# Kernel optimization log

Hardware: AMD Instinct MI355X
Metric: run time of the kernel (lower is better)

The kernel has to match this reference:

```python
import jax, jax.numpy as jnp
import numpy as np

EPS = 1e-8
THRESHOLD = 0.5  # ternary quantization threshold

IN_FEATURES = 4096
OUT_FEATURES = 4096


def setup_inputs() -> dict:
    key = jax.random.key(0)
    k_x, k_w, k_b = jax.random.split(key, 3)
    x = jax.random.normal(k_x, (2, 2048, IN_FEATURES), dtype=jnp.float32)
    # xavier_uniform init for weight (out, in)
    limit = float(np.sqrt(6.0 / (IN_FEATURES + OUT_FEATURES)))
    weight = jax.random.uniform(k_w, (OUT_FEATURES, IN_FEATURES), dtype=jnp.float32,
                                minval=-limit, maxval=limit)
    bias = jnp.zeros((OUT_FEATURES,), dtype=jnp.float32)
    return {"x": x, "weight": weight, "bias": bias}


def ternary_quantize(w):
    # scale = mean(|w|), clamped; quantize to {-1,0,1} with 0.5 threshold
    scale = jnp.maximum(jnp.mean(jnp.abs(w)), EPS)
    w_norm = w / scale
    q = jnp.sign(w_norm) * (jnp.abs(w_norm) > THRESHOLD).astype(w.dtype)
    return q, scale


def reference(x, weight, bias):
    # eval-mode forward of BitNetLinear (ternary mode, activation scaling on)
    qw, scale = ternary_quantize(weight)
    input_scale = jnp.maximum(jnp.mean(jnp.abs(x)), EPS)
    scaled_x = x / input_scale
    # F.linear: y = x @ W^T + b, with dequantized weight qw*scale
    out = jnp.einsum('bsi,oi->bso', scaled_x, qw * scale) + bias
    return out * input_scale
```

## Files before the change

### kernel.cpp

```cpp
#include <hip/hip_runtime.h>
#include <hip/hip_bf16.h>

#define AS1 __attribute__((address_space(1)))
#define AS3 __attribute__((address_space(3)))

typedef __attribute__((ext_vector_type(8))) short bfrag8;
typedef __attribute__((ext_vector_type(4))) float floatx4;

static constexpr int M = 4096, N = 4096, K = 4096;
static constexpr long long NELEM = 16777216LL;
static constexpr int PB = 1024;

__device__ __forceinline__ unsigned short f2bf(float f) {
    unsigned int u = __float_as_uint(f);
    u += 0x7FFFu + ((u >> 16) & 1u);
    return (unsigned short)(u >> 16);
}

__device__ __forceinline__ unsigned short tq(float v, float scale_f) {
    float wn = v / scale_f;
    if (fabsf(wn) > 0.5f)
        return (unsigned short)(0x3F80u | ((__float_as_uint(v) >> 16) & 0x8000u));
    return 0;
}

__device__ __forceinline__ double block_reduce(double s) {
    #pragma unroll
    for (int off = 32; off > 0; off >>= 1) s += __shfl_down(s, off, 64);
    __shared__ double part[4];
    int lane = threadIdx.x & 63, wv = threadIdx.x >> 6;
    if (lane == 0) part[wv] = s;
    __syncthreads();
    return part[0] + part[1] + part[2] + part[3];
}

__device__ __forceinline__ void block_reduce2_bcast(double& a, double& b) {
    #pragma unroll
    for (int off = 32; off > 0; off >>= 1) {
        a += __shfl_down(a, off, 64);
        b += __shfl_down(b, off, 64);
    }
    __shared__ double pa[4], pb[4];
    int lane = threadIdx.x & 63, wv = threadIdx.x >> 6;
    if (lane == 0) { pa[wv] = a; pb[wv] = b; }
    __syncthreads();
    a = pa[0] + pa[1] + pa[2] + pa[3];
    b = pb[0] + pb[1] + pb[2] + pb[3];
}

__global__ __launch_bounds__(256) void prep_reduce(
        const float* __restrict__ x, unsigned short* __restrict__ xb,
        const float* __restrict__ w,
        double* __restrict__ px, double* __restrict__ pw) {
    const int b = blockIdx.x;
    const bool isW = b >= PB;
    const int rb = isW ? b - PB : b;
    const float4* src = (const float4*)(isW ? w : x);
    const long long base = (long long)rb * 4096 + threadIdx.x;

    float4 v[16];
    #pragma unroll
    for (int i = 0; i < 16; i++) v[i] = src[base + i * 256];

    double s = 0.0;
    #pragma unroll
    for (int i = 0; i < 16; i++) {
        s += (double)fabsf(v[i].x); s += (double)fabsf(v[i].y);
        s += (double)fabsf(v[i].z); s += (double)fabsf(v[i].w);
    }

    if (!isW) {
        ushort4* xb4 = (ushort4*)xb;
        #pragma unroll
        for (int i = 0; i < 16; i++) {
            ushort4 r;
            r.x = f2bf(v[i].x); r.y = f2bf(v[i].y);
            r.z = f2bf(v[i].z); r.w = f2bf(v[i].w);
            xb4[base + i * 256] = r;
        }
    }

    double bs = block_reduce(s);
    if (threadIdx.x == 0) (isW ? pw : px)[rb] = bs;
}

__global__ __launch_bounds__(256) void quantize_w(
        const float* __restrict__ w, unsigned short* __restrict__ qb,
        const double* __restrict__ px, const double* __restrict__ pw,
        float* __restrict__ scales) {
    const int t = threadIdx.x;
    double sx = 0.0, sw = 0.0;
    #pragma unroll
    for (int i = 0; i < 4; i++) { sx += px[t + i * 256]; sw += pw[t + i * 256]; }
    block_reduce2_bcast(sx, sw);
    const float scale_w = (float)fmax(sw / (double)NELEM, 1e-8);
    const float scale_x = (float)fmax(sx / (double)NELEM, 1e-8);
    if (blockIdx.x == 0 && t == 0) { scales[0] = scale_w; scales[1] = scale_x; }

    const float4* w4 = (const float4*)w;
    ushort4* q4 = (ushort4*)qb;
    const long long base = (long long)blockIdx.x * 4096 + t;
    float4 v[16];
    #pragma unroll
    for (int i = 0; i < 16; i++) v[i] = w4[base + i * 256];
    #pragma unroll
    for (int i = 0; i < 16; i++) {
        ushort4 r;
        r.x = tq(v[i].x, scale_w); r.y = tq(v[i].y, scale_w);
        r.z = tq(v[i].z, scale_w); r.w = tq(v[i].w, scale_w);
        q4[base + i * 256] = r;
    }
}

__global__ __launch_bounds__(256) void gemm_bt(
        const unsigned short* __restrict__ A,
        const unsigned short* __restrict__ B,
        const float* __restrict__ bias,
        const float* __restrict__ scales,
        float* __restrict__ out) {
    __shared__ unsigned short lds[2 * 128 * 64];
    const char* ldsA = (const char*)lds;
    const char* ldsB = (const char*)lds + 16384;

    const int tid = threadIdx.x;
    const int lane = tid & 63;
    const int wv = tid >> 6;
    const int wm = wv & 1;
    const int wn = wv >> 1;
    const int col16 = lane & 15;
    const int quad = lane >> 4;

    const int m0 = blockIdx.y * 128;
    const int n0 = blockIdx.x * 128;

    const int srow = lane >> 3;
    const int scol = ((lane & 7) ^ srow) * 8;

    floatx4 acc[4][4];
    #pragma unroll
    for (int i = 0; i < 4; i++)
        #pragma unroll
        for (int j = 0; j < 4; j++)
            acc[i][j] = (floatx4)0.0f;

    for (int k0 = 0; k0 < K; k0 += 64) {
        #pragma unroll
        for (int j = 0; j < 4; j++) {
            const int c = wv * 4 + j;
            const int row = c * 8 + srow;
            const unsigned short* ga = A + (size_t)(m0 + row) * K + k0 + scol;
            const unsigned short* gb = B + (size_t)(n0 + row) * K + k0 + scol;
            char* la = (char*)lds + c * 1024 + lane * 16;
            char* lb = (char*)lds + 16384 + c * 1024 + lane * 16;
            __builtin_amdgcn_global_load_lds((const AS1 void*)ga, (AS3 void*)la, 16, 0, 0);
            __builtin_amdgcn_global_load_lds((const AS1 void*)gb, (AS3 void*)lb, 16, 0, 0);
        }
        __syncthreads();

        #pragma unroll
        for (int kk = 0; kk < 64; kk += 32) {
            const int kc = (kk >> 3) + quad;
            const int sw = (kc ^ (col16 & 7)) << 4;
            bfrag8 af[4], bfr[4];
            #pragma unroll
            for (int i = 0; i < 4; i++) {
                const int ra = wm * 64 + i * 16 + col16;
                const int rb = wn * 64 + i * 16 + col16;
                af[i]  = *(const bfrag8*)(ldsA + ra * 128 + sw);
                bfr[i] = *(const bfrag8*)(ldsB + rb * 128 + sw);
            }
            #pragma unroll
            for (int i = 0; i < 4; i++)
                #pragma unroll
                for (int j = 0; j < 4; j++)
                    acc[i][j] = __builtin_amdgcn_mfma_f32_16x16x32_bf16(af[i], bfr[j], acc[i][j], 0, 0, 0);
        }
        __syncthreads();
    }

    const float wscale = scales[0];
    const float iscale = scales[1];

    float bv[4];
    #pragma unroll
    for (int j = 0; j < 4; j++)
        bv[j] = bias[n0 + wn * 64 + j * 16 + col16] * iscale;

    #pragma unroll
    for (int i = 0; i < 4; i++) {
        const int mbase = m0 + wm * 64 + i * 16 + quad * 4;
        #pragma unroll
        for (int j = 0; j < 4; j++) {
            const int n = n0 + wn * 64 + j * 16 + col16;
            #pragma unroll
            for (int r = 0; r < 4; r++)
                out[(size_t)(mbase + r) * N + n] = acc[i][j][r] * wscale + bv[j];
        }
    }
}

extern "C" void kernel_launch(void* const* d_in, const int* in_sizes, int n_in,
                              void* d_out, int out_size, void* d_ws, size_t ws_size,
                              hipStream_t stream) {
    const float* x    = (const float*)d_in[0];
    const float* w    = (const float*)d_in[1];
    const float* bias = (const float*)d_in[2];
    float* out = (float*)d_out;

    char* ws = (char*)d_ws;
    float*  scales = (float*)ws;
    double* px     = (double*)(ws + 256);
    double* pw     = (double*)(ws + 256 + PB * 8);
    unsigned short* xb = (unsigned short*)(ws + 16640);
    unsigned short* qb = (unsigned short*)(ws + 16640 + (size_t)NELEM * 2);

    prep_reduce<<<2 * PB, 256, 0, stream>>>(x, xb, w, px, pw);
    quantize_w<<<PB, 256, 0, stream>>>(w, qb, px, pw, scales);

    dim3 grid(N / 128, M / 128);
    gemm_bt<<<grid, 256, 0, stream>>>(xb, qb, bias, scales, out);
}
```

Measured before the change: 329.5 us.

## Rewrite GEMM as 256x256-tile, 512-thread kernel with double-buffered LDS pipeline

Replaces the 128x128 GEMM tile with a 256x256 tile computed by 8 waves, using 128KB of LDS split into two buffers so global-to-LDS loads for the next K step overlap MFMA work on the current one. It adds an XCD-aware block index swizzle and uses setprio around MFMA bursts with explicit waitcnt and barrier control. The aim is more data reuse per loaded byte and hiding of load latency. The costs are heavy register and LDS pressure and fragile hand-written synchronization.

```diff
diff --git a/kernel.cpp b/kernel.cpp
--- a/kernel.cpp
+++ b/kernel.cpp
@@ -112,15 +112,13 @@
     }
 }
 
-__global__ __launch_bounds__(256) void gemm_bt(
+__global__ __launch_bounds__(512, 2) void gemm_bt256(
         const unsigned short* __restrict__ A,
         const unsigned short* __restrict__ B,
         const float* __restrict__ bias,
         const float* __restrict__ scales,
         float* __restrict__ out) {
-    __shared__ unsigned short lds[2 * 128 * 64];
-    const char* ldsA = (const char*)lds;
-    const char* ldsB = (const char*)lds + 16384;
+    __shared__ alignas(16) char lds[131072];
 
     const int tid = threadIdx.x;
     const int lane = tid & 63;
@@ -128,54 +126,101 @@
     const int wm = wv & 1;
     const int wn = wv >> 1;
     const int col16 = lane & 15;
-    const int quad = lane >> 4;
-
-    const int m0 = blockIdx.y * 128;
-    const int n0 = blockIdx.x * 128;
-
-    const int srow = lane >> 3;
-    const int scol = ((lane & 7) ^ srow) * 8;
-
-    floatx4 acc[4][4];
-    #pragma unroll
-    for (int i = 0; i < 4; i++)
+    const int quad  = lane >> 4;
+
+    const int bid = blockIdx.x;
+    const int swz = (bid & 7) * 32 + (bid >> 3);
+    const int bx = swz & 15;
+    const int by = swz >> 4;
+    const int m0 = by * 256;
+    const int n0 = bx * 256;
+
+    const int srow8  = lane >> 3;
+    const int schunk = (lane & 7) ^ srow8;
+    const int scol   = schunk * 8;
+
+    floatx4 acc[8][4];
+    #pragma unroll
+    for (int i = 0; i < 8; i++)
         #pragma unroll
         for (int j = 0; j < 4; j++)
             acc[i][j] = (floatx4)0.0f;
 
-    for (int k0 = 0; k0 < K; k0 += 64) {
-        #pragma unroll
-        for (int j = 0; j < 4; j++) {
-            const int c = wv * 4 + j;
-            const int row = c * 8 + srow;
-            const unsigned short* ga = A + (size_t)(m0 + row) * K + k0 + scol;
-            const unsigned short* gb = B + (size_t)(n0 + row) * K + k0 + scol;
-            char* la = (char*)lds + c * 1024 + lane * 16;
-            char* lb = (char*)lds + 16384 + c * 1024 + lane * 16;
-            __builtin_amdgcn_global_load_lds((const AS1 void*)ga, (AS3 void*)la, 16, 0, 0);
-            __builtin_amdgcn_global_load_lds((const AS1 void*)gb, (AS3 void*)lb, 16, 0, 0);
-        }
-        __syncthreads();
-
-        #pragma unroll
-        for (int kk = 0; kk < 64; kk += 32) {
-            const int kc = (kk >> 3) + quad;
-            const int sw = (kc ^ (col16 & 7)) << 4;
-            bfrag8 af[4], bfr[4];
-            #pragma unroll
-            for (int i = 0; i < 4; i++) {
-                const int ra = wm * 64 + i * 16 + col16;
-                const int rb = wn * 64 + i * 16 + col16;
-                af[i]  = *(const bfrag8*)(ldsA + ra * 128 + sw);
-                bfr[i] = *(const bfrag8*)(ldsB + rb * 128 + sw);
+    char* ldsc = (char*)lds;
+
+    auto stage4 = [&](const unsigned short* __restrict__ gmat, int base0,
+                      char* region, long long k0) {
+        #pragma unroll
+        for (int h = 0; h < 2; ++h)
+            #pragma unroll
+            for (int l = 0; l < 2; ++l) {
+                const int c = wv * 2 + l;
+                const unsigned short* g = gmat
+                    + (size_t)(base0 + h * 128 + c * 8 + srow8) * (size_t)K
+                    + (size_t)k0 + scol;
+                char* d = region + h * 16384 + c * 1024 + lane * 16;
+                __builtin_amdgcn_global_load_lds((const AS1 void*)g, (AS3 void*)d, 16, 0, 0);
             }
-            #pragma unroll
-            for (int i = 0; i < 4; i++)
+    };
+
+    stage4(A, m0, ldsc,                 0);
+    stage4(B, n0, ldsc + 32768,         0);
+    stage4(A, m0, ldsc + 65536,         64);
+    stage4(B, n0, ldsc + 65536 + 32768, 64);
+    asm volatile("s_waitcnt vmcnt(8)" ::: "memory");
+    __builtin_amdgcn_s_barrier();
+
+    auto tile_body = [&](const char* bufc, char* bufn, int t) {
+        const bool doStage = (t >= 1) && (t < 63);
+        const long long knext = (long long)(t + 1) * 64;
+        const char* bA = bufc;
+        const char* bB = bufc + 32768;
+
+        bfrag8 bf[4][2];
+        #pragma unroll
+        for (int j = 0; j < 4; ++j) {
+            const int rB = wn * 64 + j * 16 + col16;
+            #pragma unroll
+            for (int kk = 0; kk < 2; ++kk)
+                bf[j][kk] = *(const bfrag8*)(bB + rB * 128 +
+                                (((kk * 4 + quad) ^ (col16 & 7)) << 4));
+        }
+
+        #pragma unroll
+        for (int q = 0; q < 4; ++q) {
+            bfrag8 af[2][2];
+            #pragma unroll
+            for (int di = 0; di < 2; ++di) {
+                const int rA = wm * 128 + (q * 2 + di) * 16 + col16;
                 #pragma unroll
-                for (int j = 0; j < 4; j++)
-                    acc[i][j] = __builtin_amdgcn_mfma_f32_16x16x32_bf16(af[i], bfr[j], acc[i][j], 0, 0, 0);
-        }
-        __syncthreads();
+                for (int kk = 0; kk < 2; ++kk)
+                    af[di][kk] = *(const bfrag8*)(bA + rA * 128 +
+                                    (((kk * 4 + quad) ^ (col16 & 7)) << 4));
+            }
+            if (q == 0 && doStage) stage4(B, n0, bufn + 32768, knext);
+            if (q == 1 && doStage) stage4(A, m0, bufn, knext);
+
+            __builtin_amdgcn_s_barrier();
+            asm volatile("s_waitcnt lgkmcnt(0)" ::: "memory");
+            __builtin_amdgcn_s_setprio(1);
+            #pragma unroll
+            for (int di = 0; di < 2; ++di)
+                #pragma unroll
+                for (int j = 0; j < 4; ++j) {
+                    acc[q * 2 + di][j] = __builtin_amdgcn_mfma_f32_16x16x32_bf16(
+                        af[di][0], bf[j][0], acc[q * 2 + di][j], 0, 0, 0);
+                    acc[q * 2 + di][j] = __builtin_amdgcn_mfma_f32_16x16x32_bf16(
+                        af[di][1], bf[j][1], acc[q * 2 + di][j], 0, 0, 0);
+                }
+            __builtin_amdgcn_s_setprio(0);
+            if (q == 3) asm volatile("s_waitcnt vmcnt(0)" ::: "memory");
+            __builtin_amdgcn_s_barrier();
+        }
+    };
+
+    for (int t2 = 0; t2 < 32; ++t2) {
+        tile_body(ldsc,         ldsc + 65536, 2 * t2);
+        tile_body(ldsc + 65536, ldsc,         2 * t2 + 1);
     }
 
     const float wscale = scales[0];
@@ -183,17 +228,17 @@
 
     float bv[4];
     #pragma unroll
-    for (int j = 0; j < 4; j++)
+    for (int j = 0; j < 4; ++j)
         bv[j] = bias[n0 + wn * 64 + j * 16 + col16] * iscale;
 
     #pragma unroll
-    for (int i = 0; i < 4; i++) {
-        const int mbase = m0 + wm * 64 + i * 16 + quad * 4;
-        #pragma unroll
-        for (int j = 0; j < 4; j++) {
+    for (int i = 0; i < 8; ++i) {
+        const int mbase = m0 + wm * 128 + i * 16 + quad * 4;
+        #pragma unroll
+        for (int j = 0; j < 4; ++j) {
             const int n = n0 + wn * 64 + j * 16 + col16;
             #pragma unroll
-            for (int r = 0; r < 4; r++)
+            for (int r = 0; r < 4; ++r)
                 out[(size_t)(mbase + r) * N + n] = acc[i][j][r] * wscale + bv[j];
         }
     }
@@ -217,6 +262,5 @@
     prep_reduce<<<2 * PB, 256, 0, stream>>>(x, xb, w, px, pw);
     quantize_w<<<PB, 256, 0, stream>>>(w, qb, px, pw, scales);
 
-    dim3 grid(N / 128, M / 128);
-    gemm_bt<<<grid, 256, 0, stream>>>(xb, qb, bias, scales, out);
-}
+    gemm_bt256<<<dim3(256), 512, 0, stream>>>(xb, qb, bias, scales, out);
+}
```

Result: slower. 339.3 us (+3.0%).
